# Kernel optimization log

Hardware: AMD Instinct MI355X
Metric: run time of the kernel (lower is better)

## Reference

```python
import jax, jax.numpy as jnp
import numpy as np

L, E, D = 4, 512, 256   # layers, model dim (=2*D bidirectional), per-direction hidden
T, B = 100, 1000
EPS = 1e-5

def _layernorm(x, g, b):
    m = x.mean(-1, keepdims=True)
    v = x.var(-1, keepdims=True)
    return (x - m) / jnp.sqrt(v + EPS) * g + b

def _dir_scan(U, vf, vr, bf, br):
    # U: (T, B, 4, D) pre-projected gates; SRU elementwise recurrence over time.
    def step(c, u):
        f = jax.nn.sigmoid(u[:, 1] + vf * c + bf)
        c2 = f * c + (1.0 - f) * u[:, 0]
        r = jax.nn.sigmoid(u[:, 2] + vr * c2 + br)
        h = r * c2 + (1.0 - r) * u[:, 3]   # highway with projected residual u3
        return c2, h
    c0 = jnp.zeros((U.shape[1], U.shape[-1]), U.dtype)
    _, H = jax.lax.scan(step, c0, U)
    return H

def setup_inputs() -> dict:
    key = jax.random.key(0)
    ks = jax.random.split(key, 6)
    return {
        "sentence": jax.random.normal(ks[0], (T, B, E), jnp.float32),
        "sru_W": jax.random.normal(ks[1], (L, 2, E, 4 * D), jnp.float32) / np.float32(np.sqrt(E)),
        "sru_v": jax.random.normal(ks[2], (L, 2, 2, D), jnp.float32) * 0.05,
        "sru_b": jnp.zeros((L, 2, 2, D), jnp.float32),
        "ln_g": jnp.ones((L, E), jnp.float32),
        "ln_b": jnp.zeros((L, E), jnp.float32),
        "W1": jax.random.normal(ks[3], (E, E), jnp.float32) / np.float32(np.sqrt(E)),
        "b1": jnp.zeros((E,), jnp.float32),
        "bn_g": jnp.ones((E,), jnp.float32),
        "bn_b": jnp.zeros((E,), jnp.float32),
        "bn_mean": jnp.zeros((E,), jnp.float32),
        "bn_var": jnp.ones((E,), jnp.float32),
        "W2": jax.random.normal(ks[4], (E, 4), jnp.float32) / np.float32(np.sqrt(E)),
        "b2": jnp.zeros((4,), jnp.float32),
    }

def reference(sentence, sru_W, sru_v, sru_b, ln_g, ln_b, W1, b1, bn_g, bn_b, bn_mean, bn_var, W2, b2):
    x = sentence  # (T, B, E)
    for l in range(L):
        xl = _layernorm(x, ln_g[l], ln_b[l])
        # batched projection for both directions: (2, T, B, 4, D)
        U = jnp.einsum('tbi,dik->dtbk', xl, sru_W[l]).reshape(2, T, B, 4, D)
        Hf = _dir_scan(U[0], sru_v[l, 0, 0], sru_v[l, 0, 1], sru_b[l, 0, 0], sru_b[l, 0, 1])
        Hb = _dir_scan(U[1][::-1], sru_v[l, 1, 0], sru_v[l, 1, 1], sru_b[l, 1, 0], sru_b[l, 1, 1])[::-1]
        x = jnp.concatenate([Hf, Hb], axis=-1)  # (T, B, E)
    # head on flattened tokens (eval mode: dropout off, BN uses running stats)
    h = x.reshape(-1, E) @ W1 + b1
    h = (h - bn_mean) / jnp.sqrt(bn_var + EPS) * bn_g + bn_b
    h = jax.nn.relu(h)
    logits = h @ W2 + b2  # (T*B, 4)
    return jax.nn.log_softmax(logits, axis=-1)
```

## Files before the change

### kernel.cpp

```cpp
#include <hip/hip_runtime.h>
#include <stdint.h>

#define T_DIM 100
#define B_DIM 1000
#define E_DIM 512
#define D_DIM 256
#define L_DIM 4
#define M_TOK (T_DIM * B_DIM)
#define M_PAD 100096
#define K_DIM 512
#define MT128 782

typedef unsigned short u16;
typedef __bf16 bf16x8 __attribute__((ext_vector_type(8)));
typedef float f32x4 __attribute__((ext_vector_type(4)));
typedef unsigned short ushort8 __attribute__((ext_vector_type(8)));
typedef unsigned short ushort4v __attribute__((ext_vector_type(4)));

__device__ __forceinline__ u16 f2bf(float f) {
  unsigned int u = __builtin_bit_cast(unsigned int, f);
  u += 0x7fffu + ((u >> 16) & 1u);
  return (u16)(u >> 16);
}
__device__ __forceinline__ float bf2f(u16 h) {
  unsigned int u = ((unsigned int)h) << 16;
  return __builtin_bit_cast(float, u);
}

__device__ __forceinline__ void gld16(const u16* g, u16* l) {
  __builtin_amdgcn_global_load_lds(
      (const __attribute__((address_space(1))) unsigned int*)g,
      (__attribute__((address_space(3))) unsigned int*)l, 16, 0, 0);
}

__global__ void transpose_cast(const float* __restrict__ in, u16* __restrict__ out,
                               int R, int C, int perm4) {
  __shared__ float t[32][33];
  const int s = blockIdx.z;
  const float* ib = in + (size_t)s * R * C;
  u16* ob = out + (size_t)s * R * C;
  const int c0 = blockIdx.x * 32, r0 = blockIdx.y * 32;
  const int tx = threadIdx.x, ty = threadIdx.y;
#pragma unroll
  for (int j = 0; j < 4; ++j)
    t[ty + j * 8][tx] = ib[(size_t)(r0 + ty + j * 8) * C + c0 + tx];
  __syncthreads();
#pragma unroll
  for (int j = 0; j < 4; ++j) {
    const int cc = c0 + ty + j * 8;
    const int n = perm4 ? ((cc & 255) * 4 + (cc >> 8)) : cc;
    ob[(size_t)n * R + r0 + tx] = f2bf(t[tx][ty + j * 8]);
  }
}

__global__ __launch_bounds__(256) void zero_pad(u16* __restrict__ xl) {
  const int i = blockIdx.x * 256 + threadIdx.x;
  ushort8 z = {0, 0, 0, 0, 0, 0, 0, 0};
  *(ushort8*)(xl + (size_t)M_TOK * 512 + (size_t)i * 8) = z;
}

template <typename TI>
__global__ __launch_bounds__(256) void ln_cast_kernel(
    const TI* __restrict__ x, const float* __restrict__ g,
    const float* __restrict__ b, u16* __restrict__ out) {
  const int wid = threadIdx.x >> 6, lane = threadIdx.x & 63;
  const int row = blockIdx.x * 4 + wid;
  float xe[8];
  if constexpr (sizeof(TI) == 4) {
    const float* xr = (const float*)x + (size_t)row * E_DIM + lane * 8;
    const float4 a = *(const float4*)xr;
    const float4 c = *(const float4*)(xr + 4);
    xe[0] = a.x; xe[1] = a.y; xe[2] = a.z; xe[3] = a.w;
    xe[4] = c.x; xe[5] = c.y; xe[6] = c.z; xe[7] = c.w;
  } else {
    const u16* xr = (const u16*)x + (size_t)row * E_DIM + lane * 8;
    const ushort8 hv = *(const ushort8*)xr;
#pragma unroll
    for (int u = 0; u < 8; ++u) xe[u] = bf2f(hv[u]);
  }
  float s = 0.f, q = 0.f;
#pragma unroll
  for (int u = 0; u < 8; ++u) { s += xe[u]; q += xe[u] * xe[u]; }
#pragma unroll
  for (int off = 32; off; off >>= 1) {
    s += __shfl_xor(s, off, 64);
    q += __shfl_xor(q, off, 64);
  }
  const float mean = s * (1.0f / 512.0f);
  const float var = q * (1.0f / 512.0f) - mean * mean;
  const float rstd = rsqrtf(var + 1e-5f);
  const float4 g0 = *(const float4*)(g + lane * 8);
  const float4 g1 = *(const float4*)(g + lane * 8 + 4);
  const float4 b0 = *(const float4*)(b + lane * 8);
  const float4 b1v = *(const float4*)(b + lane * 8 + 4);
  float ge[8] = {g0.x, g0.y, g0.z, g0.w, g1.x, g1.y, g1.z, g1.w};
  float be[8] = {b0.x, b0.y, b0.z, b0.w, b1v.x, b1v.y, b1v.z, b1v.w};
  ushort8 o;
#pragma unroll
  for (int u = 0; u < 8; ++u)
    o[u] = f2bf((xe[u] - mean) * rstd * ge[u] + be[u]);
  *(ushort8*)(out + (size_t)row * E_DIM + lane * 8) = o;
}

__global__ __launch_bounds__(256, 4) void gemm_bf16(
    const u16* __restrict__ A, const u16* __restrict__ B, u16* __restrict__ C,
    int N, int nc_shift, int ncol_shift) {
  __shared__ u16 As[2][4096];
  __shared__ u16 Bs[2][4096];

  const int bid = blockIdx.x;
  const int xcd = bid & 7;
  const int kk = bid >> 3;
  const int cix = kk & ((1 << nc_shift) - 1);
  const int jj = kk >> nc_shift;
  const int mt = xcd + 8 * jj;
  if (mt >= MT128) return;
  const int z = cix >> ncol_shift;
  const int n0 = (cix & ((1 << ncol_shift) - 1)) << 7;

  const int tid = threadIdx.x;
  const int wave = tid >> 6, lane = tid & 63;
  const int wm = wave >> 1, wn = wave & 1;

  const int r_l = lane >> 2;
  const int c_ld = (lane & 3) ^ ((lane >> 3) & 3);
  const u16* Ag = A + ((size_t)mt * 128 + wave * 32 + r_l) * K_DIM + c_ld * 8;
  const u16* Bg = B + ((size_t)z * N + n0 + wave * 32 + r_l) * K_DIM + c_ld * 8;

  auto STAGE = [&](int t) {
    u16* al = &As[t & 1][wave * 1024];
    u16* bl = &Bs[t & 1][wave * 1024];
    const u16* ag = Ag + t * 32;
    const u16* bg = Bg + t * 32;
    gld16(ag, al);
    gld16(ag + 16 * K_DIM, al + 512);
    gld16(bg, bl);
    gld16(bg + 16 * K_DIM, bl + 512);
  };

  STAGE(0);

  f32x4 acc[4][4] = {};
  const int rA = lane & 15;
  const int sw = ((lane >> 4) ^ ((rA >> 1) & 3)) * 8;
  const int offA = (wm * 64 + rA) * 32 + sw;
  const int offB = (wn * 64 + rA) * 32 + sw;

  asm volatile("s_waitcnt vmcnt(0)" ::: "memory");
  asm volatile("s_barrier" ::: "memory");

#pragma unroll
  for (int t = 0; t < 16; ++t) {
    if (t < 15) STAGE(t + 1);
    const u16* Ab = As[t & 1];
    const u16* Bb = Bs[t & 1];
    bf16x8 af[4], bfr[4];
#pragma unroll
    for (int mi = 0; mi < 4; ++mi)
      af[mi] = *(const bf16x8*)&Ab[offA + mi * 512];
#pragma unroll
    for (int ni = 0; ni < 4; ++ni)
      bfr[ni] = *(const bf16x8*)&Bs[t & 1][offB + ni * 512];
#pragma unroll
    for (int mi = 0; mi < 4; ++mi)
#pragma unroll
      for (int ni = 0; ni < 4; ++ni)
        acc[mi][ni] = __builtin_amdgcn_mfma_f32_16x16x32_bf16(
            af[mi], bfr[ni], acc[mi][ni], 0, 0, 0);
    (void)Bb;
    if (t < 15) {
      asm volatile("s_waitcnt vmcnt(0)" ::: "memory");
      asm volatile("s_barrier" ::: "memory");
    }
  }

  u16* Cb = C + (size_t)z * M_PAD * N;
  const int rr = (lane >> 4) * 4;
  const int cc = lane & 15;
#pragma unroll
  for (int mi = 0; mi < 4; ++mi) {
#pragma unroll
    for (int ni = 0; ni < 4; ++ni) {
      const size_t row = (size_t)mt * 128 + wm * 64 + mi * 16 + rr;
      const int col = n0 + wn * 64 + ni * 16 + cc;
#pragma unroll
      for (int r = 0; r < 4; ++r)
        Cb[(row + r) * N + col] = f2bf(acc[mi][ni][r]);
    }
  }
}

__global__ __launch_bounds__(256) void sru_scan(const u16* __restrict__ U,
                                                const float* __restrict__ v,
                                                const float* __restrict__ bb,
                                                u16* __restrict__ xout) {
  const int d = threadIdx.x;
  const int b = blockIdx.x;
  const int dir = blockIdx.y;
  const float vf = v[(dir * 2 + 0) * 256 + d];
  const float vr = v[(dir * 2 + 1) * 256 + d];
  const float bf = bb[(dir * 2 + 0) * 256 + d];
  const float br = bb[(dir * 2 + 1) * 256 + d];
  const u16* Ud = U + (size_t)dir * M_PAD * 1024;
  float c = 0.f;
  for (int s = 0; s < T_DIM; ++s) {
    const int t = dir ? (T_DIM - 1 - s) : s;
    const size_t base = ((size_t)t * B_DIM + b) * 1024 + d * 4;
    const ushort4v uv = *(const ushort4v*)(Ud + base);
    const float u0 = bf2f(uv.x);
    const float u1 = bf2f(uv.y);
    const float u2 = bf2f(uv.z);
    const float u3 = bf2f(uv.w);
    const float f = 1.f / (1.f + __expf(-(u1 + vf * c + bf)));
    c = f * c + (1.f - f) * u0;
    const float r = 1.f / (1.f + __expf(-(u2 + vr * c + br)));
    const float h = r * c + (1.f - r) * u3;
    xout[((size_t)t * B_DIM + b) * 512 + dir * 256 + d] = f2bf(h);
  }
}

__global__ __launch_bounds__(256) void head_kernel(
    const u16* __restrict__ h, const float* __restrict__ b1,
    const float* __restrict__ bn_g, const float* __restrict__ bn_b,
    const float* __restrict__ bn_mean, const float* __restrict__ bn_var,
    const float* __restrict__ W2, const float* __restrict__ b2,
    float* __restrict__ out) {
  const int wid = threadIdx.x >> 6, lane = threadIdx.x & 63;
  const int row = blockIdx.x * 4 + wid;
  const u16* hr = h + (size_t)row * E_DIM + lane * 8;
  const ushort8 hv = *(const ushort8*)hr;
  float s0 = 0.f, s1 = 0.f, s2 = 0.f, s3 = 0.f;
  const int j0 = lane * 8;
#pragma unroll
  for (int u = 0; u < 8; ++u) {
    const int j = j0 + u;
    const float hb = bf2f(hv[u]) + b1[j];
    float hn = (hb - bn_mean[j]) * rsqrtf(bn_var[j] + 1e-5f) * bn_g[j] + bn_b[j];
    hn = fmaxf(hn, 0.f);
    const float4 w = *(const float4*)(W2 + j * 4);
    s0 += hn * w.x; s1 += hn * w.y; s2 += hn * w.z; s3 += hn * w.w;
  }
#pragma unroll
  for (int off = 32; off; off >>= 1) {
    s0 += __shfl_xor(s0, off, 64);
    s1 += __shfl_xor(s1, off, 64);
    s2 += __shfl_xor(s2, off, 64);
    s3 += __shfl_xor(s3, off, 64);
  }
  if (lane == 0) {
    const float4 bv = *(const float4*)b2;
    const float l0 = s0 + bv.x, l1 = s1 + bv.y, l2 = s2 + bv.z, l3 = s3 + bv.w;
    const float mx = fmaxf(fmaxf(l0, l1), fmaxf(l2, l3));
    const float lse =
        mx + logf(__expf(l0 - mx) + __expf(l1 - mx) + __expf(l2 - mx) + __expf(l3 - mx));
    float4 o = {l0 - lse, l1 - lse, l2 - lse, l3 - lse};
    *(float4*)(out + (size_t)row * 4) = o;
  }
}

extern "C" void kernel_launch(void* const* d_in, const int* in_sizes, int n_in,
                              void* d_out, int out_size, void* d_ws, size_t ws_size,
                              hipStream_t stream) {
  const float* sentence = (const float*)d_in[0];
  const float* sru_W = (const float*)d_in[1];
  const float* sru_v = (const float*)d_in[2];
  const float* sru_b = (const float*)d_in[3];
  const float* ln_g = (const float*)d_in[4];
  const float* ln_b = (const float*)d_in[5];
  const float* W1 = (const float*)d_in[6];
  const float* b1 = (const float*)d_in[7];
  const float* bn_g = (const float*)d_in[8];
  const float* bn_b = (const float*)d_in[9];
  const float* bn_mean = (const float*)d_in[10];
  const float* bn_var = (const float*)d_in[11];
  const float* W2 = (const float*)d_in[12];
  const float* b2 = (const float*)d_in[13];

  char* ws = (char*)d_ws;
  const size_t XL_OFF = 0;
  const size_t X_OFF = XL_OFF + (size_t)M_PAD * 512 * 2;
  const size_t U_OFF = X_OFF + (size_t)M_TOK * 512 * 2;
  const size_t WT_OFF = U_OFF + (size_t)2 * M_PAD * 1024 * 2;
  const size_t W1T_OFF = WT_OFF + (size_t)8 * 512 * 1024 * 2;
  u16* xl = (u16*)(ws + XL_OFF);
  u16* x_buf = (u16*)(ws + X_OFF);
  u16* U = (u16*)(ws + U_OFF);
  u16* WT = (u16*)(ws + WT_OFF);
  u16* W1T = (u16*)(ws + W1T_OFF);
  u16* hbuf = U;

  transpose_cast<<<dim3(32, 16, 8), dim3(32, 8), 0, stream>>>(sru_W, WT, 512, 1024, 1);
  transpose_cast<<<dim3(16, 16, 1), dim3(32, 8), 0, stream>>>(W1, W1T, 512, 512, 0);
  zero_pad<<<24, 256, 0, stream>>>(xl);

  for (int l = 0; l < L_DIM; ++l) {
    if (l == 0)
      ln_cast_kernel<float><<<M_TOK / 4, 256, 0, stream>>>(
          sentence, ln_g, ln_b, xl);
    else
      ln_cast_kernel<u16><<<M_TOK / 4, 256, 0, stream>>>(
          x_buf, ln_g + l * 512, ln_b + l * 512, xl);
    gemm_bf16<<<dim3(8 * 16 * 98), 256, 0, stream>>>(
        xl, WT + (size_t)l * 2 * 1024 * 512, U, 1024, 4, 3);
    u16* xo = (l == L_DIM - 1) ? xl : x_buf;
    sru_scan<<<dim3(1000, 2), 256, 0, stream>>>(U, sru_v + l * 1024,
                                                sru_b + l * 1024, xo);
  }
  gemm_bf16<<<dim3(8 * 4 * 98), 256, 0, stream>>>(xl, W1T, hbuf, 512, 2, 2);
  head_kernel<<<M_TOK / 4, 256, 0, stream>>>(hbuf, b1, bn_g, bn_b, bn_mean,
                                             bn_var, W2, b2, (float*)d_out);
}
```

Measured before the change: 2.174 ms.

## Load GEMM B fragments directly from global and prefetch next scan step

The GEMM kernel no longer stages the weight (B) tile through LDS. Each wave reads its B MFMA fragments straight from global memory, which halves LDS traffic and footprint, and the A-tile prefetch is now issued after those loads. The SRU scan kernel software-prefetches the next timestep's gate values so global latency overlaps the recurrence math. The risk is that direct global B loads are redundant across the two wm waves, rely on cache hits, and add latency that the vmcnt(0) wait before the barrier now exposes.

```diff
diff --git a/kernel.cpp b/kernel.cpp
--- a/kernel.cpp
+++ b/kernel.cpp
@@ -106,7 +106,6 @@
     const u16* __restrict__ A, const u16* __restrict__ B, u16* __restrict__ C,
     int N, int nc_shift, int ncol_shift) {
   __shared__ u16 As[2][4096];
-  __shared__ u16 Bs[2][4096];
 
   const int bid = blockIdx.x;
   const int xcd = bid & 7;
@@ -125,49 +124,45 @@
   const int r_l = lane >> 2;
   const int c_ld = (lane & 3) ^ ((lane >> 3) & 3);
   const u16* Ag = A + ((size_t)mt * 128 + wave * 32 + r_l) * K_DIM + c_ld * 8;
-  const u16* Bg = B + ((size_t)z * N + n0 + wave * 32 + r_l) * K_DIM + c_ld * 8;
-
-  auto STAGE = [&](int t) {
+
+  auto STAGE_A = [&](int t) {
     u16* al = &As[t & 1][wave * 1024];
-    u16* bl = &Bs[t & 1][wave * 1024];
     const u16* ag = Ag + t * 32;
-    const u16* bg = Bg + t * 32;
     gld16(ag, al);
     gld16(ag + 16 * K_DIM, al + 512);
-    gld16(bg, bl);
-    gld16(bg + 16 * K_DIM, bl + 512);
   };
 
-  STAGE(0);
+  const int rA = lane & 15;
+  const int ch = lane >> 4;
+  const int sw = (ch ^ ((rA >> 1) & 3)) * 8;
+  const int offA = (wm * 64 + rA) * 32 + sw;
+  const u16* Bg = B + ((size_t)z * N + n0 + wn * 64 + rA) * K_DIM + ch * 8;
+
+  STAGE_A(0);
 
   f32x4 acc[4][4] = {};
-  const int rA = lane & 15;
-  const int sw = ((lane >> 4) ^ ((rA >> 1) & 3)) * 8;
-  const int offA = (wm * 64 + rA) * 32 + sw;
-  const int offB = (wn * 64 + rA) * 32 + sw;
 
   asm volatile("s_waitcnt vmcnt(0)" ::: "memory");
   asm volatile("s_barrier" ::: "memory");
 
 #pragma unroll
   for (int t = 0; t < 16; ++t) {
-    if (t < 15) STAGE(t + 1);
     const u16* Ab = As[t & 1];
-    const u16* Bb = Bs[t & 1];
-    bf16x8 af[4], bfr[4];
+    bf16x8 af[4], bcur[4];
 #pragma unroll
     for (int mi = 0; mi < 4; ++mi)
       af[mi] = *(const bf16x8*)&Ab[offA + mi * 512];
 #pragma unroll
     for (int ni = 0; ni < 4; ++ni)
-      bfr[ni] = *(const bf16x8*)&Bs[t & 1][offB + ni * 512];
+      bcur[ni] = *(const bf16x8*)(Bg + (size_t)ni * 16 * K_DIM + t * 32);
+    __builtin_amdgcn_sched_barrier(0);
+    if (t < 15) STAGE_A(t + 1);
 #pragma unroll
     for (int mi = 0; mi < 4; ++mi)
 #pragma unroll
       for (int ni = 0; ni < 4; ++ni)
         acc[mi][ni] = __builtin_amdgcn_mfma_f32_16x16x32_bf16(
-            af[mi], bfr[ni], acc[mi][ni], 0, 0, 0);
-    (void)Bb;
+            af[mi], bcur[ni], acc[mi][ni], 0, 0, 0);
     if (t < 15) {
       asm volatile("s_waitcnt vmcnt(0)" ::: "memory");
       asm volatile("s_barrier" ::: "memory");
@@ -203,10 +198,15 @@
   const float br = bb[(dir * 2 + 1) * 256 + d];
   const u16* Ud = U + (size_t)dir * M_PAD * 1024;
   float c = 0.f;
+  const int t0 = dir ? (T_DIM - 1) : 0;
+  const long step = dir ? -(long)(B_DIM * 1024) : (long)(B_DIM * 1024);
+  const size_t base0 = ((size_t)t0 * B_DIM + b) * 1024 + d * 4;
+  ushort4v uv = *(const ushort4v*)(Ud + base0);
   for (int s = 0; s < T_DIM; ++s) {
+    ushort4v nx = uv;
+    if (s + 1 < T_DIM)
+      nx = *(const ushort4v*)(Ud + (size_t)((long)base0 + step * (s + 1)));
     const int t = dir ? (T_DIM - 1 - s) : s;
-    const size_t base = ((size_t)t * B_DIM + b) * 1024 + d * 4;
-    const ushort4v uv = *(const ushort4v*)(Ud + base);
     const float u0 = bf2f(uv.x);
     const float u1 = bf2f(uv.y);
     const float u2 = bf2f(uv.z);
@@ -216,6 +216,7 @@
     const float r = 1.f / (1.f + __expf(-(u2 + vr * c + br)));
     const float h = r * c + (1.f - r) * u3;
     xout[((size_t)t * B_DIM + b) * 512 + dir * 256 + d] = f2bf(h);
+    uv = nx;
   }
 }
 
```

After: 2.923 ms. 34.5% more time.

## Fuse SRU scan with next layer's LayerNorm via shared-memory staging

Applied to the files above, without the earlier changes.

A new kernel runs both scan directions for one batch element in a 512-thread block. It keeps all 100 timesteps of h in shared memory and then applies the next layer's LayerNorm directly, writing the bf16 normalized input. This removes the separate LN kernel and the round trip of the intermediate x buffer through global memory for layers 0-2. It also adds software prefetching of upcoming U loads, five steps deep in the fused kernel and one step in the plain scan. The cost is about 104KB of shared memory per block, which limits occupancy to one or two blocks per CU and may hurt latency hiding in the serial scan.

```diff
diff --git a/kernel.cpp b/kernel.cpp
--- a/kernel.cpp
+++ b/kernel.cpp
@@ -59,25 +59,15 @@
   *(ushort8*)(xl + (size_t)M_TOK * 512 + (size_t)i * 8) = z;
 }
 
-template <typename TI>
 __global__ __launch_bounds__(256) void ln_cast_kernel(
-    const TI* __restrict__ x, const float* __restrict__ g,
+    const float* __restrict__ x, const float* __restrict__ g,
     const float* __restrict__ b, u16* __restrict__ out) {
   const int wid = threadIdx.x >> 6, lane = threadIdx.x & 63;
   const int row = blockIdx.x * 4 + wid;
-  float xe[8];
-  if constexpr (sizeof(TI) == 4) {
-    const float* xr = (const float*)x + (size_t)row * E_DIM + lane * 8;
-    const float4 a = *(const float4*)xr;
-    const float4 c = *(const float4*)(xr + 4);
-    xe[0] = a.x; xe[1] = a.y; xe[2] = a.z; xe[3] = a.w;
-    xe[4] = c.x; xe[5] = c.y; xe[6] = c.z; xe[7] = c.w;
-  } else {
-    const u16* xr = (const u16*)x + (size_t)row * E_DIM + lane * 8;
-    const ushort8 hv = *(const ushort8*)xr;
-#pragma unroll
-    for (int u = 0; u < 8; ++u) xe[u] = bf2f(hv[u]);
-  }
+  const float* xr = x + (size_t)row * E_DIM + lane * 8;
+  const float4 a = *(const float4*)xr;
+  const float4 c = *(const float4*)(xr + 4);
+  float xe[8] = {a.x, a.y, a.z, a.w, c.x, c.y, c.z, c.w};
   float s = 0.f, q = 0.f;
 #pragma unroll
   for (int u = 0; u < 8; ++u) { s += xe[u]; q += xe[u] * xe[u]; }
@@ -153,7 +143,6 @@
   for (int t = 0; t < 16; ++t) {
     if (t < 15) STAGE(t + 1);
     const u16* Ab = As[t & 1];
-    const u16* Bb = Bs[t & 1];
     bf16x8 af[4], bfr[4];
 #pragma unroll
     for (int mi = 0; mi < 4; ++mi)
@@ -167,7 +156,6 @@
       for (int ni = 0; ni < 4; ++ni)
         acc[mi][ni] = __builtin_amdgcn_mfma_f32_16x16x32_bf16(
             af[mi], bfr[ni], acc[mi][ni], 0, 0, 0);
-    (void)Bb;
     if (t < 15) {
       asm volatile("s_waitcnt vmcnt(0)" ::: "memory");
       asm volatile("s_barrier" ::: "memory");
@@ -187,6 +175,84 @@
       for (int r = 0; r < 4; ++r)
         Cb[(row + r) * N + col] = f2bf(acc[mi][ni][r]);
     }
+  }
+}
+
+__global__ __launch_bounds__(512) void sru_scan_ln(
+    const u16* __restrict__ U, const float* __restrict__ v,
+    const float* __restrict__ bb, const float* __restrict__ g,
+    const float* __restrict__ b, u16* __restrict__ xl) {
+  __shared__ u16 hl[T_DIM * 520];
+  const int tid = threadIdx.x;
+  const int d = tid & 255;
+  const int dir = tid >> 8;
+  const int bidx = blockIdx.x;
+  const float vf = v[(dir * 2 + 0) * 256 + d];
+  const float vr = v[(dir * 2 + 1) * 256 + d];
+  const float bf = bb[(dir * 2 + 0) * 256 + d];
+  const float br = bb[(dir * 2 + 1) * 256 + d];
+  const u16* Ud = U + (size_t)dir * M_PAD * 1024;
+  const int t0 = dir ? (T_DIM - 1) : 0;
+  const long step = dir ? -(long)(B_DIM * 1024) : (long)(B_DIM * 1024);
+  const size_t base0 = ((size_t)t0 * B_DIM + bidx) * 1024 + d * 4;
+
+  auto LD = [&](int idx) {
+    return *(const ushort4v*)(Ud + (size_t)((long)base0 + step * (long)idx));
+  };
+
+  ushort4v pf[5];
+#pragma unroll
+  for (int j = 0; j < 5; ++j) pf[j] = LD(j);
+
+  float c = 0.f;
+  for (int sb = 0; sb < T_DIM; sb += 5) {
+#pragma unroll
+    for (int j = 0; j < 5; ++j) {
+      const int s = sb + j;
+      const ushort4v uv = pf[j];
+      if (sb + 5 + j < T_DIM) pf[j] = LD(sb + 5 + j);
+      const float u0 = bf2f(uv.x);
+      const float u1 = bf2f(uv.y);
+      const float u2 = bf2f(uv.z);
+      const float u3 = bf2f(uv.w);
+      const float f = 1.f / (1.f + __expf(-(u1 + vf * c + bf)));
+      c = f * c + (1.f - f) * u0;
+      const float r = 1.f / (1.f + __expf(-(u2 + vr * c + br)));
+      const float h = r * c + (1.f - r) * u3;
+      const int t = dir ? (T_DIM - 1 - s) : s;
+      hl[t * 520 + dir * 256 + d] = f2bf(h);
+    }
+  }
+  __syncthreads();
+
+  const int lane = tid & 63, w = tid >> 6;
+  const float4 g0 = *(const float4*)(g + lane * 8);
+  const float4 g1 = *(const float4*)(g + lane * 8 + 4);
+  const float4 b0 = *(const float4*)(b + lane * 8);
+  const float4 b1v = *(const float4*)(b + lane * 8 + 4);
+  const float ge[8] = {g0.x, g0.y, g0.z, g0.w, g1.x, g1.y, g1.z, g1.w};
+  const float be[8] = {b0.x, b0.y, b0.z, b0.w, b1v.x, b1v.y, b1v.z, b1v.w};
+  for (int row = w; row < T_DIM; row += 8) {
+    const ushort8 hv = *(const ushort8*)&hl[row * 520 + lane * 8];
+    float xe[8];
+#pragma unroll
+    for (int u = 0; u < 8; ++u) xe[u] = bf2f(hv[u]);
+    float s = 0.f, q = 0.f;
+#pragma unroll
+    for (int u = 0; u < 8; ++u) { s += xe[u]; q += xe[u] * xe[u]; }
+#pragma unroll
+    for (int off = 32; off; off >>= 1) {
+      s += __shfl_xor(s, off, 64);
+      q += __shfl_xor(q, off, 64);
+    }
+    const float mean = s * (1.0f / 512.0f);
+    const float var = q * (1.0f / 512.0f) - mean * mean;
+    const float rstd = rsqrtf(var + 1e-5f);
+    ushort8 o;
+#pragma unroll
+    for (int u = 0; u < 8; ++u)
+      o[u] = f2bf((xe[u] - mean) * rstd * ge[u] + be[u]);
+    *(ushort8*)(xl + ((size_t)row * B_DIM + bidx) * 512 + lane * 8) = o;
   }
 }
 
@@ -203,10 +269,15 @@
   const float br = bb[(dir * 2 + 1) * 256 + d];
   const u16* Ud = U + (size_t)dir * M_PAD * 1024;
   float c = 0.f;
+  const int t0 = dir ? (T_DIM - 1) : 0;
+  const long step = dir ? -(long)(B_DIM * 1024) : (long)(B_DIM * 1024);
+  const size_t base0 = ((size_t)t0 * B_DIM + b) * 1024 + d * 4;
+  ushort4v uv = *(const ushort4v*)(Ud + base0);
   for (int s = 0; s < T_DIM; ++s) {
+    ushort4v nx = uv;
+    if (s + 1 < T_DIM)
+      nx = *(const ushort4v*)(Ud + (size_t)((long)base0 + step * (s + 1)));
     const int t = dir ? (T_DIM - 1 - s) : s;
-    const size_t base = ((size_t)t * B_DIM + b) * 1024 + d * 4;
-    const ushort4v uv = *(const ushort4v*)(Ud + base);
     const float u0 = bf2f(uv.x);
     const float u1 = bf2f(uv.y);
     const float u2 = bf2f(uv.z);
@@ -216,6 +287,7 @@
     const float r = 1.f / (1.f + __expf(-(u2 + vr * c + br)));
     const float h = r * c + (1.f - r) * u3;
     xout[((size_t)t * B_DIM + b) * 512 + dir * 256 + d] = f2bf(h);
+    uv = nx;
   }
 }
 
@@ -283,7 +355,6 @@
   const size_t WT_OFF = U_OFF + (size_t)2 * M_PAD * 1024 * 2;
   const size_t W1T_OFF = WT_OFF + (size_t)8 * 512 * 1024 * 2;
   u16* xl = (u16*)(ws + XL_OFF);
-  u16* x_buf = (u16*)(ws + X_OFF);
   u16* U = (u16*)(ws + U_OFF);
   u16* WT = (u16*)(ws + WT_OFF);
   u16* W1T = (u16*)(ws + W1T_OFF);
@@ -293,18 +364,19 @@
   transpose_cast<<<dim3(16, 16, 1), dim3(32, 8), 0, stream>>>(W1, W1T, 512, 512, 0);
   zero_pad<<<24, 256, 0, stream>>>(xl);
 
+  ln_cast_kernel<<<M_TOK / 4, 256, 0, stream>>>(sentence, ln_g, ln_b, xl);
+
   for (int l = 0; l < L_DIM; ++l) {
-    if (l == 0)
-      ln_cast_kernel<float><<<M_TOK / 4, 256, 0, stream>>>(
-          sentence, ln_g, ln_b, xl);
-    else
-      ln_cast_kernel<u16><<<M_TOK / 4, 256, 0, stream>>>(
-          x_buf, ln_g + l * 512, ln_b + l * 512, xl);
     gemm_bf16<<<dim3(8 * 16 * 98), 256, 0, stream>>>(
         xl, WT + (size_t)l * 2 * 1024 * 512, U, 1024, 4, 3);
-    u16* xo = (l == L_DIM - 1) ? xl : x_buf;
-    sru_scan<<<dim3(1000, 2), 256, 0, stream>>>(U, sru_v + l * 1024,
-                                                sru_b + l * 1024, xo);
+    if (l < L_DIM - 1) {
+      sru_scan_ln<<<B_DIM, 512, 0, stream>>>(
+          U, sru_v + l * 1024, sru_b + l * 1024,
+          ln_g + (l + 1) * 512, ln_b + (l + 1) * 512, xl);
+    } else {
+      sru_scan<<<dim3(B_DIM, 2), 256, 0, stream>>>(
+          U, sru_v + l * 1024, sru_b + l * 1024, xl);
+    }
   }
   gemm_bf16<<<dim3(8 * 4 * 98), 256, 0, stream>>>(xl, W1T, hbuf, 512, 2, 2);
   head_kernel<<<M_TOK / 4, 256, 0, stream>>>(hbuf, b1, bn_g, bn_b, bn_mean,
```

New measurement: 2.137 ms. About the same (-1.7%).
